# Optimization experiments

Measured on AMD Instinct MI355X. Metric: run time of the kernel, lower is better.

## Reference

```python
import jax, jax.numpy as jnp
import numpy as np

EPS_BN = 1e-5
K_NN = 5


def _curvature(x, k=K_NN):
    # x: [B, P, 3] -> concat inverse mean kNN distance -> [B, P, 4]
    def per_sample(pts):  # [P, 3]
        sq = jnp.sum(pts * pts, axis=1)
        d2 = sq[:, None] + sq[None, :] - 2.0 * (pts @ pts.T)
        dist = jnp.sqrt(jnp.maximum(d2, 0.0))  # [P, P], matches torch.cdist p=2
        neg_vals, _ = jax.lax.top_k(-dist, k + 1)  # k+1 smallest distances
        dists = -neg_vals[:, 1:]  # drop self (distance 0)
        dmean = jnp.mean(dists, axis=1, keepdims=True)  # [P, 1]
        return 1.0 / (1e-8 + dmean)
    curv = jax.vmap(per_sample)(x)  # [B, P, 1]
    return jnp.concatenate([x, curv], axis=2)


def _bn(h, g, b, axes):
    # BatchNorm (training mode, batch statistics), biased variance like torch
    m = jnp.mean(h, axis=axes, keepdims=True)
    v = jnp.var(h, axis=axes, keepdims=True)
    return (h - m) / jnp.sqrt(v + EPS_BN) * g + b


def setup_inputs() -> dict:
    key = jax.random.key(0)
    ks = jax.random.split(key, 16)
    B, P, OUTDIM = 32, 2048, 40

    def rn(k, shape, scale=0.05):
        return jax.random.normal(k, shape, dtype=jnp.float32) * scale

    return {
        "x": jax.random.normal(ks[0], (B, P, 3), dtype=jnp.float32),
        # 1x1 Conv1d weights stored as [out_ch, in_ch]
        "conv1_w": rn(ks[1], (64, 4)), "conv1_b": rn(ks[2], (64,)),
        "bn1_g": jnp.ones((64,), jnp.float32), "bn1_b": jnp.zeros((64,), jnp.float32),
        "conv2_w": rn(ks[3], (128, 64)), "conv2_b": rn(ks[4], (128,)),
        "bn2_g": jnp.ones((128,), jnp.float32), "bn2_b": jnp.zeros((128,), jnp.float32),
        "conv3_w": rn(ks[5], (1024, 128)), "conv3_b": rn(ks[6], (1024,)),
        "bn3_g": jnp.ones((1024,), jnp.float32), "bn3_b": jnp.zeros((1024,), jnp.float32),
        "fc1_w": rn(ks[7], (512, 1024)), "fc1_b": rn(ks[8], (512,)),
        "bnf1_g": jnp.ones((512,), jnp.float32), "bnf1_b": jnp.zeros((512,), jnp.float32),
        "fc2_w": rn(ks[9], (256, 512)), "fc2_b": rn(ks[10], (256,)),
        "bnf2_g": jnp.ones((256,), jnp.float32), "bnf2_b": jnp.zeros((256,), jnp.float32),
        # outdim separate Linear(256,1) layers stacked into one [OUTDIM, 256] matrix
        "out_w": rn(ks[11], (OUTDIM, 256)), "out_b": rn(ks[12], (OUTDIM,)),
    }


def reference(x, conv1_w, conv1_b, bn1_g, bn1_b, conv2_w, conv2_b, bn2_g, bn2_b,
              conv3_w, conv3_b, bn3_g, bn3_b, fc1_w, fc1_b, bnf1_g, bnf1_b,
              fc2_w, fc2_b, bnf2_g, bnf2_b, out_w, out_b):
    h = _curvature(x)  # [B, P, 4]
    # feature_layer1: Conv1d(4,64,1)+BN+ReLU; 1x1 conv == per-point matmul
    h = jax.nn.relu(_bn(h @ conv1_w.T + conv1_b, bn1_g, bn1_b, (0, 1)))
    # feature_layer2: Conv1d(64,128,1)+BN+ReLU, Conv1d(128,1024,1)+BN+ReLU
    h = jax.nn.relu(_bn(h @ conv2_w.T + conv2_b, bn2_g, bn2_b, (0, 1)))
    h = jax.nn.relu(_bn(h @ conv3_w.T + conv3_b, bn3_g, bn3_b, (0, 1)))
    h = jnp.max(h, axis=1)  # global max pool over points -> [B, 1024]
    # shared_layer
    h = jax.nn.relu(_bn(h @ fc1_w.T + fc1_b, bnf1_g, bnf1_b, (0,)))
    h = jax.nn.relu(_bn(h @ fc2_w.T + fc2_b, bnf2_g, bnf2_b, (0,)))
    logits = h @ out_w.T + out_b  # concatenated per-class Linear(256,1) heads
    return jax.nn.log_softmax(logits, axis=1)
```

## Files before the change

kernel.cpp:

```cpp
#include <hip/hip_runtime.h>
#include <hip/hip_bf16.h>
#include <math.h>

#define EPS_BN 1e-5f

constexpr int BATCH = 32;
constexpr int NPTS  = 2048;
constexpr int BP    = BATCH * NPTS;

using s16x8 = __attribute__((ext_vector_type(8))) short;
using u32x4 = __attribute__((ext_vector_type(4))) unsigned;
using f32x4 = __attribute__((ext_vector_type(4))) float;

static __device__ __forceinline__ unsigned short f2bf(float f) {
  union { float f; unsigned u; } x{f};
  unsigned r = x.u + 0x7fffu + ((x.u >> 16) & 1u);
  return (unsigned short)(r >> 16);
}
static __device__ __forceinline__ float bf2f(unsigned short s) {
  union { unsigned u; float f; } x;
  x.u = ((unsigned)s) << 16;
  return x.f;
}
static __device__ __forceinline__ unsigned pk2bf(float lo, float hi) {
  __hip_bfloat162 t = __float22bfloat162_rn(float2{lo, hi});
  unsigned r;
  __builtin_memcpy(&r, &t, 4);
  return r;
}

static __device__ __forceinline__ void gload_lds16(const void* g, void* l) {
  __builtin_amdgcn_global_load_lds((const __attribute__((address_space(1))) void*)g,
                                   (__attribute__((address_space(3))) void*)l, 16, 0, 0);
}

static __device__ __forceinline__ float wave_reduce_add(float v) {
#pragma unroll
  for (int off = 32; off > 0; off >>= 1) v += __shfl_xor(v, off);
  return v;
}

static __device__ __forceinline__ void ins6(float (&nn)[6], float c) {
  float b0 = fminf(nn[0], c);
  float b1 = __builtin_amdgcn_fmed3f(c, nn[1], nn[0]);
  float b2 = __builtin_amdgcn_fmed3f(c, nn[2], nn[1]);
  float b3 = __builtin_amdgcn_fmed3f(c, nn[3], nn[2]);
  float b4 = __builtin_amdgcn_fmed3f(c, nn[4], nn[3]);
  float b5 = __builtin_amdgcn_fmed3f(c, nn[5], nn[4]);
  nn[0] = b0; nn[1] = b1; nn[2] = b2; nn[3] = b3; nn[4] = b4; nn[5] = b5;
}

constexpr int CH = 260;
__global__ __launch_bounds__(256) void curv_kernel(const float* __restrict__ x,
                                                   float* __restrict__ feat) {
  __shared__ float sx[8 * CH], sy[8 * CH], sz[8 * CH], sh[8 * CH];
  int b = blockIdx.y;
  const float* xb = x + (size_t)b * NPTS * 3;
  int tid = threadIdx.x;
#pragma unroll
  for (int k = 0; k < 8; k++) {
    int i = k * 256 + tid;
    float qx = xb[i * 3 + 0], qy = xb[i * 3 + 1], qz = xb[i * 3 + 2];
    sx[k * CH + tid] = qx;
    sy[k * CH + tid] = qy;
    sz[k * CH + tid] = qz;
    sh[k * CH + tid] = 0.5f * (qx * qx + qy * qy + qz * qz);
  }
  __syncthreads();
  int row = blockIdx.x * 32 + (tid >> 3);
  int sub = tid & 7;
  float px = sx[(row >> 8) * CH + (row & 255)];
  float py = sy[(row >> 8) * CH + (row & 255)];
  float pz = sz[(row >> 8) * CH + (row & 255)];
  float nn[6];
#pragma unroll
  for (int j = 0; j < 6; j++) nn[j] = 3.4e38f;
  const float4* cx = (const float4*)(sx + sub * CH);
  const float4* cy = (const float4*)(sy + sub * CH);
  const float4* cz = (const float4*)(sz + sub * CH);
  const float4* chq = (const float4*)(sh + sub * CH);
  for (int j = 0; j < 64; j++) {
    float4 qx = cx[j], qy = cy[j], qz = cz[j], qh = chq[j];
    ins6(nn, fmaf(-px, qx.x, fmaf(-py, qy.x, fmaf(-pz, qz.x, qh.x))));
    ins6(nn, fmaf(-px, qx.y, fmaf(-py, qy.y, fmaf(-pz, qz.y, qh.y))));
    ins6(nn, fmaf(-px, qx.z, fmaf(-py, qy.z, fmaf(-pz, qz.z, qh.z))));
    ins6(nn, fmaf(-px, qx.w, fmaf(-py, qy.w, fmaf(-pz, qz.w, qh.w))));
  }
#pragma unroll
  for (int m = 1; m <= 4; m <<= 1) {
    float other[6];
#pragma unroll
    for (int k = 0; k < 6; k++) other[k] = __shfl_xor(nn[k], m);
#pragma unroll
    for (int k = 0; k < 6; k++) ins6(nn, other[k]);
  }
  if (sub == 0) {
    float p2 = px * px + py * py + pz * pz;
    float dm = 0.f;
#pragma unroll
    for (int i = 1; i < 6; i++) dm += sqrtf(fmaxf(fmaf(2.f, nn[i], p2), 0.f));
    dm *= 0.2f;
    float curv = 1.0f / (1e-8f + dm);
    size_t o = ((size_t)b * NPTS + row) * 4;
    feat[o + 0] = px;
    feat[o + 1] = py;
    feat[o + 2] = pz;
    feat[o + 3] = curv;
  }
}

__global__ __launch_bounds__(256) void gemm1s_kernel(const float* __restrict__ feat,
                                                     const float* __restrict__ w,
                                                     const float* __restrict__ bias,
                                                     unsigned short* __restrict__ z1bf,
                                                     float* __restrict__ part) {
  __shared__ float wT[4 * 64];
  int tid = threadIdx.x;
  { int k = tid >> 6, c = tid & 63; wT[k * 64 + c] = w[c * 4 + k]; }
  __syncthreads();
  int col = tid & 63, rg = tid >> 6;
  int row0 = blockIdx.x * 64;
  float w0 = wT[col], w1 = wT[64 + col], w2v = wT[128 + col], w3 = wT[192 + col];
  float bb = bias[col];
  float s = 0.f, q = 0.f;
  for (int i = 0; i < 16; i++) {
    int row = row0 + i * 4 + rg;
    const float4 f = *(const float4*)(feat + (size_t)row * 4);
    float acc = bb + f.x * w0 + f.y * w1 + f.z * w2v + f.w * w3;
    s += acc;
    q += acc * acc;
    z1bf[(size_t)row * 64 + col] = f2bf(acc);
  }
  __shared__ float ls[256], lq[256];
  ls[tid] = s; lq[tid] = q;
  __syncthreads();
  if (tid < 64) {
    float ss = 0.f, qq = 0.f;
#pragma unroll
    for (int i = 0; i < 4; i++) { ss += ls[i * 64 + tid]; qq += lq[i * 64 + tid]; }
    part[((size_t)blockIdx.x * 64 + tid) * 2 + 0] = ss;
    part[((size_t)blockIdx.x * 64 + tid) * 2 + 1] = qq;
  }
}

template <int C, int P>
__global__ __launch_bounds__(256) void bnfinP_kernel(const float* __restrict__ part,
                                                     const float* __restrict__ g,
                                                     const float* __restrict__ be,
                                                     float* __restrict__ scale,
                                                     float* __restrict__ shift) {
  int c = blockIdx.x, tid = threadIdx.x;
  float s = 0.f, q = 0.f;
  for (int i = tid; i < P; i += 256) {
    s += part[((size_t)i * C + c) * 2 + 0];
    q += part[((size_t)i * C + c) * 2 + 1];
  }
  __shared__ float ls[256], lq[256];
  ls[tid] = s; lq[tid] = q;
  __syncthreads();
  for (int off = 128; off > 0; off >>= 1) {
    if (tid < off) { ls[tid] += ls[tid + off]; lq[tid] += lq[tid + off]; }
    __syncthreads();
  }
  if (tid == 0) {
    float m = ls[0] * (1.0f / 65536.0f);
    float v = lq[0] * (1.0f / 65536.0f) - m * m;
    float a = g[c] / sqrtf(v + EPS_BN);
    scale[c] = a;
    shift[c] = be[c] - m * a;
  }
}

__global__ __launch_bounds__(256) void gemm2_mfma_kernel(const unsigned short* __restrict__ z1bf,
                                                         const float* __restrict__ s1,
                                                         const float* __restrict__ h1,
                                                         const float* __restrict__ w2,
                                                         const float* __restrict__ bias2,
                                                         unsigned short* __restrict__ z2bf,
                                                         float* __restrict__ part2) {
  __shared__ char lds[33280];
  float* ls1 = (float*)(lds + 32768);
  float* lh1 = ls1 + 64;
  int tid = threadIdx.x;
  int row0 = blockIdx.x * 128;
  if (tid < 64) { ls1[tid] = s1[tid]; lh1[tid] = h1[tid]; }

  s16x8 araw[4];
  float4 b0[4], b1[4];
#pragma unroll
  for (int i = 0; i < 4; i++) {
    int L = tid + 256 * i;
    araw[i] = *(const s16x8*)(z1bf + (size_t)row0 * 64 + (size_t)L * 8);
    int crow = L >> 3, k0 = (L & 7) * 8;
    b0[i] = *(const float4*)(w2 + (size_t)crow * 64 + k0);
    b1[i] = *(const float4*)(w2 + (size_t)crow * 64 + k0 + 4);
  }
  __syncthreads();

#pragma unroll
  for (int i = 0; i < 4; i++) {
    int L = tid + 256 * i;
    int row = L >> 3, grp = L & 7, k0 = grp * 8;
    float4 sA = *(const float4*)(ls1 + k0);
    float4 sB = *(const float4*)(ls1 + k0 + 4);
    float4 hA = *(const float4*)(lh1 + k0);
    float4 hB = *(const float4*)(lh1 + k0 + 4);
    float v0 = fmaxf(bf2f((unsigned short)araw[i][0]) * sA.x + hA.x, 0.f);
    float v1 = fmaxf(bf2f((unsigned short)araw[i][1]) * sA.y + hA.y, 0.f);
    float v2 = fmaxf(bf2f((unsigned short)araw[i][2]) * sA.z + hA.z, 0.f);
    float v3 = fmaxf(bf2f((unsigned short)araw[i][3]) * sA.w + hA.w, 0.f);
    float v4 = fmaxf(bf2f((unsigned short)araw[i][4]) * sB.x + hB.x, 0.f);
    float v5 = fmaxf(bf2f((unsigned short)araw[i][5]) * sB.y + hB.y, 0.f);
    float v6 = fmaxf(bf2f((unsigned short)araw[i][6]) * sB.z + hB.z, 0.f);
    float v7 = fmaxf(bf2f((unsigned short)araw[i][7]) * sB.w + hB.w, 0.f);
    u32x4 pa = {pk2bf(v0, v1), pk2bf(v2, v3), pk2bf(v4, v5), pk2bf(v6, v7)};
    *(u32x4*)(lds + row * 128 + ((grp ^ (row & 7)) << 4)) = pa;
    u32x4 pb = {pk2bf(b0[i].x, b0[i].y), pk2bf(b0[i].z, b0[i].w),
                pk2bf(b1[i].x, b1[i].y), pk2bf(b1[i].z, b1[i].w)};
    *(u32x4*)(lds + 16384 + row * 128 + ((grp ^ (row & 7)) << 4)) = pb;
  }
  __syncthreads();

  int w = tid >> 6, lane = tid & 63;
  int wm = w >> 1, wn = w & 1;
  int lrow = lane & 15, lg = lane >> 4;
  int sw = (lrow & 7) << 4;
  f32x4 acc[4][4] = {};
#pragma unroll
  for (int kstep = 0; kstep < 2; kstep++) {
    s16x8 a[4], bfr[4];
#pragma unroll
    for (int m = 0; m < 4; m++) {
      int row = wm * 64 + m * 16 + lrow;
      int byte = row * 128 + ((kstep * 64 + lg * 16) ^ sw);
      a[m] = *(const s16x8*)(lds + byte);
    }
#pragma unroll
    for (int n = 0; n < 4; n++) {
      int col = wn * 64 + n * 16 + lrow;
      int byte = 16384 + col * 128 + ((kstep * 64 + lg * 16) ^ sw);
      bfr[n] = *(const s16x8*)(lds + byte);
    }
#pragma unroll
    for (int m = 0; m < 4; m++)
#pragma unroll
      for (int n = 0; n < 4; n++)
        acc[m][n] = __builtin_amdgcn_mfma_f32_16x16x32_bf16(a[m], bfr[n], acc[m][n], 0, 0, 0);
  }
  __syncthreads();

  float* sS = (float*)lds;
  float* sQ = sS + 256;
#pragma unroll
  for (int n = 0; n < 4; n++) {
    int col = wn * 64 + n * 16 + lrow;
    float bb = bias2[col];
    float s = 0.f, q = 0.f;
#pragma unroll
    for (int m = 0; m < 4; m++) {
#pragma unroll
      for (int r = 0; r < 4; r++) {
        float v = acc[m][n][r] + bb;
        s += v;
        q += v * v;
        int row = row0 + wm * 64 + m * 16 + lg * 4 + r;
        z2bf[(size_t)row * 128 + col] = f2bf(v);
      }
    }
    s += __shfl_xor(s, 16); s += __shfl_xor(s, 32);
    q += __shfl_xor(q, 16); q += __shfl_xor(q, 32);
    if (lane < 16) {
      int cidx = wn * 64 + n * 16 + lane;
      sS[wm * 128 + cidx] = s;
      sQ[wm * 128 + cidx] = q;
    }
  }
  __syncthreads();
  if (tid < 128) {
    part2[((size_t)blockIdx.x * 128 + tid) * 2 + 0] = sS[tid] + sS[128 + tid];
    part2[((size_t)blockIdx.x * 128 + tid) * 2 + 1] = sQ[tid] + sQ[128 + tid];
  }
}

__global__ __launch_bounds__(256) void wconv_kernel(const float* __restrict__ w,
                                                    unsigned short* __restrict__ wbf) {
  int g = blockIdx.x * 256 + threadIdx.x;
  const float4 v = ((const float4*)w)[g];
  unsigned short o0 = f2bf(v.x), o1 = f2bf(v.y), o2 = f2bf(v.z), o3 = f2bf(v.w);
  unsigned short* d = wbf + (size_t)g * 4;
  d[0] = o0; d[1] = o1; d[2] = o2; d[3] = o3;
}

__global__ __launch_bounds__(256) void gemm3_mfma_kernel(const unsigned short* __restrict__ z2bf,
                                                         const float* __restrict__ s2,
                                                         const float* __restrict__ h2,
                                                         const unsigned short* __restrict__ wbf,
                                                         const float* __restrict__ bias3,
                                                         float* __restrict__ pS,
                                                         float* __restrict__ pQ,
                                                         float* __restrict__ pMx,
                                                         float* __restrict__ pMn) {
  __shared__ char lds[70656];
  float* ls2 = (float*)(lds + 69632);
  float* lh2 = ls2 + 128;
  int tid = threadIdx.x;
  int w = tid >> 6, lane = tid & 63;
  int bid = blockIdx.x;
  int rblk = (bid & 7) * 64 + (bid >> 3);
  int row0 = rblk * 128;

  if (tid < 128) { ls2[tid] = s2[tid]; lh2[tid] = h2[tid]; }
  s16x8 araw[8];
#pragma unroll
  for (int i = 0; i < 8; i++) {
    int L = tid + 256 * i;
    int row = L >> 4, gc = L & 15;
    araw[i] = *(const s16x8*)(z2bf + (size_t)(row0 + row) * 128 + gc * 8);
  }
  __syncthreads();
#pragma unroll
  for (int i = 0; i < 8; i++) {
    int L = tid + 256 * i;
    int row = L >> 4, gc = L & 15, k0 = gc * 8;
    float4 sA = *(const float4*)(ls2 + k0);
    float4 sB = *(const float4*)(ls2 + k0 + 4);
    float4 hA = *(const float4*)(lh2 + k0);
    float4 hB = *(const float4*)(lh2 + k0 + 4);
    float v0 = fmaxf(bf2f((unsigned short)araw[i][0]) * sA.x + hA.x, 0.f);
    float v1 = fmaxf(bf2f((unsigned short)araw[i][1]) * sA.y + hA.y, 0.f);
    float v2 = fmaxf(bf2f((unsigned short)araw[i][2]) * sA.z + hA.z, 0.f);
    float v3 = fmaxf(bf2f((unsigned short)araw[i][3]) * sA.w + hA.w, 0.f);
    float v4 = fmaxf(bf2f((unsigned short)araw[i][4]) * sB.x + hB.x, 0.f);
    float v5 = fmaxf(bf2f((unsigned short)araw[i][5]) * sB.y + hB.y, 0.f);
    float v6 = fmaxf(bf2f((unsigned short)araw[i][6]) * sB.z + hB.z, 0.f);
    float v7 = fmaxf(bf2f((unsigned short)araw[i][7]) * sB.w + hB.w, 0.f);
    u32x4 pa = {pk2bf(v0, v1), pk2bf(v2, v3), pk2bf(v4, v5), pk2bf(v6, v7)};
    *(u32x4*)(lds + row * 256 + ((gc ^ (row & 7)) << 4)) = pa;
  }

  int wm = w >> 1, wn = w & 1;
  int lrow = lane & 15, lg = lane >> 4;
  int sw = (lrow & 7) << 4;
  float* sS = (float*)(lds + 65536);
  float* sQ = sS + 256;
  float* sMx = sQ + 256;
  float* sMn = sMx + 256;

  for (int cblk = 0; cblk < 8; cblk++) {
    int col0 = cblk * 128;
#pragma unroll
    for (int i = 0; i < 8; i++) {
      int ldsoff = w * 8192 + i * 1024;
      int lin = ldsoff + lane * 16;
      int row = lin >> 8;
      int gc = (lin >> 4) & 15;
      int gcl = gc ^ (row & 7);
      gload_lds16(wbf + (size_t)(col0 + row) * 128 + gcl * 8, &lds[32768 + ldsoff]);
    }
    __syncthreads();

    f32x4 acc[4][4] = {};
#pragma unroll
    for (int kstep = 0; kstep < 4; kstep++) {
      s16x8 a[4], b[4];
#pragma unroll
      for (int m = 0; m < 4; m++) {
        int row = wm * 64 + m * 16 + lrow;
        int byte = row * 256 + ((kstep * 64 + lg * 16) ^ sw);
        a[m] = *(const s16x8*)(lds + byte);
      }
#pragma unroll
      for (int n = 0; n < 4; n++) {
        int col = wn * 64 + n * 16 + lrow;
        int byte = 32768 + col * 256 + ((kstep * 64 + lg * 16) ^ sw);
        b[n] = *(const s16x8*)(lds + byte);
      }
#pragma unroll
      for (int m = 0; m < 4; m++)
#pragma unroll
        for (int n = 0; n < 4; n++)
          acc[m][n] = __builtin_amdgcn_mfma_f32_16x16x32_bf16(a[m], b[n], acc[m][n], 0, 0, 0);
    }

#pragma unroll
    for (int n = 0; n < 4; n++) {
      float bb = bias3[col0 + wn * 64 + n * 16 + lrow];
      float s = 0.f, q = 0.f, mx = -3.4e38f, mn = 3.4e38f;
#pragma unroll
      for (int m = 0; m < 4; m++)
#pragma unroll
        for (int r = 0; r < 4; r++) {
          float v = acc[m][n][r] + bb;
          s += v;
          q += v * v;
          mx = fmaxf(mx, v);
          mn = fminf(mn, v);
        }
      s += __shfl_xor(s, 16); s += __shfl_xor(s, 32);
      q += __shfl_xor(q, 16); q += __shfl_xor(q, 32);
      mx = fmaxf(mx, __shfl_xor(mx, 16)); mx = fmaxf(mx, __shfl_xor(mx, 32));
      mn = fminf(mn, __shfl_xor(mn, 16)); mn = fminf(mn, __shfl_xor(mn, 32));
      if (lane < 16) {
        int cidx = wn * 64 + n * 16 + lane;
        sS[wm * 128 + cidx] = s;
        sQ[wm * 128 + cidx] = q;
        sMx[wm * 128 + cidx] = mx;
        sMn[wm * 128 + cidx] = mn;
      }
    }
    __syncthreads();
    if (tid < 128) {
      size_t o = (size_t)rblk * 1024 + col0 + tid;
      pS[o] = sS[tid] + sS[128 + tid];
      pQ[o] = sQ[tid] + sQ[128 + tid];
      pMx[o] = fmaxf(sMx[tid], sMx[128 + tid]);
      pMn[o] = fminf(sMn[tid], sMn[128 + tid]);
    }
    __syncthreads();
  }
}

__global__ __launch_bounds__(256) void bn3fin_pool_kernel(const float* __restrict__ pS,
                                                          const float* __restrict__ pQ,
                                                          const float* __restrict__ pMx,
                                                          const float* __restrict__ pMn,
                                                          const float* __restrict__ g,
                                                          const float* __restrict__ be,
                                                          float* __restrict__ pooled) {
  int tid = threadIdx.x;
  int chl = tid & 15, grp = tid >> 4;
  int c = blockIdx.x * 16 + chl;
  float s = 0.f, q = 0.f;
  for (int i = grp; i < 512; i += 16) {
    s += pS[(size_t)i * 1024 + c];
    q += pQ[(size_t)i * 1024 + c];
  }
  __shared__ float ls[256], lq[256], sa[16], sc[16];
  ls[chl * 16 + grp] = s;
  lq[chl * 16 + grp] = q;
  __syncthreads();
  if (tid < 16) {
    float ss = 0.f, qq = 0.f;
#pragma unroll
    for (int i = 0; i < 16; i++) { ss += ls[tid * 16 + i]; qq += lq[tid * 16 + i]; }
    float m = ss * (1.0f / 65536.0f);
    float v = qq * (1.0f / 65536.0f) - m * m;
    float a = g[blockIdx.x * 16 + tid] / sqrtf(v + EPS_BN);
    sa[tid] = a;
    sc[tid] = be[blockIdx.x * 16 + tid] - m * a;
  }
  __syncthreads();
  for (int idx = tid; idx < 512; idx += 256) {
    int b = idx >> 4, l = idx & 15;
    int cc = blockIdx.x * 16 + l;
    float mx = -3.4e38f, mn = 3.4e38f;
    for (int i = 0; i < 16; i++) {
      mx = fmaxf(mx, pMx[(size_t)(b * 16 + i) * 1024 + cc]);
      mn = fminf(mn, pMn[(size_t)(b * 16 + i) * 1024 + cc]);
    }
    float a = sa[l];
    float v = (a > 0.f) ? (a * mx + sc[l]) : (a * mn + sc[l]);
    pooled[(size_t)b * 1024 + cc] = fmaxf(v, 0.f);
  }
}

__global__ __launch_bounds__(256) void fc1_kernel(const float* __restrict__ pooled,
                                                  const float* __restrict__ w,
                                                  const float* __restrict__ bias,
                                                  float* __restrict__ zf1) {
  int gw = blockIdx.x * 4 + (threadIdx.x >> 6);
  int lane = threadIdx.x & 63;
  int b = gw >> 9, o = gw & 511;
  const float4* pr = (const float4*)(pooled + (size_t)b * 1024);
  const float4* wr = (const float4*)(w + (size_t)o * 1024);
  float acc = 0.f;
#pragma unroll
  for (int i = 0; i < 4; i++) {
    int k = lane + i * 64;
    float4 p = pr[k], q = wr[k];
    acc += p.x * q.x + p.y * q.y + p.z * q.z + p.w * q.w;
  }
  acc = wave_reduce_add(acc);
  if (lane == 0) zf1[gw] = acc + bias[o];
}

__global__ __launch_bounds__(256) void statsF_kernel(const float* __restrict__ z,
                                                     const float* __restrict__ g,
                                                     const float* __restrict__ be, int C,
                                                     float* __restrict__ scale,
                                                     float* __restrict__ shift) {
  int c = blockIdx.x * 256 + threadIdx.x;
  if (c >= C) return;
  float s = 0.f, q = 0.f;
  for (int b = 0; b < 32; b++) {
    float v = z[(size_t)b * C + c];
    s += v;
    q += v * v;
  }
  float m = s * (1.0f / 32.0f);
  float v = q * (1.0f / 32.0f) - m * m;
  float a = g[c] / sqrtf(v + EPS_BN);
  scale[c] = a;
  shift[c] = be[c] - m * a;
}

__global__ __launch_bounds__(256) void fc2_kernel(const float* __restrict__ zf1,
                                                  const float* __restrict__ sf1,
                                                  const float* __restrict__ hf1,
                                                  const float* __restrict__ w,
                                                  const float* __restrict__ bias,
                                                  float* __restrict__ zf2) {
  int gw = blockIdx.x * 4 + (threadIdx.x >> 6);
  int lane = threadIdx.x & 63;
  int b = gw >> 8, o = gw & 255;
  const float4* zr = (const float4*)(zf1 + (size_t)b * 512);
  const float4* sr = (const float4*)sf1;
  const float4* hr = (const float4*)hf1;
  const float4* wr = (const float4*)(w + (size_t)o * 512);
  float acc = 0.f;
#pragma unroll
  for (int i = 0; i < 2; i++) {
    int k = lane + i * 64;
    float4 z = zr[k], s = sr[k], h = hr[k], q = wr[k];
    float v0 = fmaxf(z.x * s.x + h.x, 0.f);
    float v1 = fmaxf(z.y * s.y + h.y, 0.f);
    float v2 = fmaxf(z.z * s.z + h.z, 0.f);
    float v3 = fmaxf(z.w * s.w + h.w, 0.f);
    acc += v0 * q.x + v1 * q.y + v2 * q.z + v3 * q.w;
  }
  acc = wave_reduce_add(acc);
  if (lane == 0) zf2[gw] = acc + bias[o];
}

__global__ __launch_bounds__(256) void head_kernel(const float* __restrict__ zf2,
                                                   const float* __restrict__ gf2,
                                                   const float* __restrict__ bef2,
                                                   const float* __restrict__ w,
                                                   const float* __restrict__ bias,
                                                   float* __restrict__ out) {
  int b = blockIdx.x, tid = threadIdx.x;
  int wv = tid >> 6, lane = tid & 63;
  __shared__ float ssf[256], shf[256], lg[40], red[2];
  {
    float s = 0.f, q = 0.f;
    for (int bb = 0; bb < 32; bb++) {
      float v = zf2[(size_t)bb * 256 + tid];
      s += v;
      q += v * v;
    }
    float m = s * (1.0f / 32.0f);
    float var = q * (1.0f / 32.0f) - m * m;
    float a = gf2[tid] / sqrtf(var + EPS_BN);
    ssf[tid] = a;
    shf[tid] = bef2[tid] - m * a;
  }
  __syncthreads();
  float4 z = ((const float4*)(zf2 + (size_t)b * 256))[lane];
  float4 s = ((const float4*)ssf)[lane];
  float4 h = ((const float4*)shf)[lane];
  float v0 = fmaxf(z.x * s.x + h.x, 0.f);
  float v1 = fmaxf(z.y * s.y + h.y, 0.f);
  float v2 = fmaxf(z.z * s.z + h.z, 0.f);
  float v3 = fmaxf(z.w * s.w + h.w, 0.f);
  for (int r = 0; r < 10; r++) {
    int o = wv * 10 + r;
    float4 q = ((const float4*)(w + (size_t)o * 256))[lane];
    float a = v0 * q.x + v1 * q.y + v2 * q.z + v3 * q.w;
    a = wave_reduce_add(a);
    if (lane == 0) lg[o] = a + bias[o];
  }
  __syncthreads();
  if (tid == 0) {
    float mx = -3.4e38f;
    for (int i = 0; i < 40; i++) mx = fmaxf(mx, lg[i]);
    float sum = 0.f;
    for (int i = 0; i < 40; i++) sum += expf(lg[i] - mx);
    red[0] = mx;
    red[1] = logf(sum);
  }
  __syncthreads();
  if (tid < 40) out[(size_t)b * 40 + tid] = lg[tid] - red[0] - red[1];
}

extern "C" void kernel_launch(void* const* d_in, const int* in_sizes, int n_in,
                              void* d_out, int out_size, void* d_ws, size_t ws_size,
                              hipStream_t stream) {
  const float* x    = (const float*)d_in[0];
  const float* c1w  = (const float*)d_in[1];
  const float* c1b  = (const float*)d_in[2];
  const float* g1   = (const float*)d_in[3];
  const float* be1  = (const float*)d_in[4];
  const float* c2w  = (const float*)d_in[5];
  const float* c2b  = (const float*)d_in[6];
  const float* g2   = (const float*)d_in[7];
  const float* be2  = (const float*)d_in[8];
  const float* c3w  = (const float*)d_in[9];
  const float* c3b  = (const float*)d_in[10];
  const float* g3   = (const float*)d_in[11];
  const float* be3  = (const float*)d_in[12];
  const float* f1w  = (const float*)d_in[13];
  const float* f1b  = (const float*)d_in[14];
  const float* gf1  = (const float*)d_in[15];
  const float* bef1 = (const float*)d_in[16];
  const float* f2w  = (const float*)d_in[17];
  const float* f2b  = (const float*)d_in[18];
  const float* gf2  = (const float*)d_in[19];
  const float* bef2 = (const float*)d_in[20];
  const float* ow   = (const float*)d_in[21];
  const float* ob   = (const float*)d_in[22];
  float* out = (float*)d_out;

  float* W = (float*)d_ws;
  float* feat   = W;
  float* pS     = feat + 262144;
  float* pQ     = pS + 524288;
  float* pMx    = pQ + 524288;
  float* pMn    = pMx + 524288;
  float* part   = pMn + 524288;
  float* part2  = part + 131072;
  float* pooled = part2 + 131072;
  float* zf1    = pooled + 32768;
  float* zf2    = zf1 + 16384;
  float* s1     = zf2 + 8192;
  float* h1     = s1 + 64;
  float* s2     = h1 + 64;
  float* h2     = s2 + 128;
  float* sf1    = h2 + 128;
  float* hf1    = sf1 + 512;
  unsigned short* wbf  = (unsigned short*)(hf1 + 512);
  unsigned short* z1bf = wbf + 131072;
  unsigned short* z2bf = z1bf + (size_t)BP * 64;

  wconv_kernel<<<128, 256, 0, stream>>>(c3w, wbf);
  curv_kernel<<<dim3(64, 32), 256, 0, stream>>>(x, feat);
  gemm1s_kernel<<<1024, 256, 0, stream>>>(feat, c1w, c1b, z1bf, part);
  bnfinP_kernel<64, 1024><<<64, 256, 0, stream>>>(part, g1, be1, s1, h1);
  gemm2_mfma_kernel<<<512, 256, 0, stream>>>(z1bf, s1, h1, c2w, c2b, z2bf, part2);
  bnfinP_kernel<128, 512><<<128, 256, 0, stream>>>(part2, g2, be2, s2, h2);
  gemm3_mfma_kernel<<<512, 256, 0, stream>>>(z2bf, s2, h2, wbf, c3b, pS, pQ, pMx, pMn);
  bn3fin_pool_kernel<<<64, 256, 0, stream>>>(pS, pQ, pMx, pMn, g3, be3, pooled);
  fc1_kernel<<<4096, 256, 0, stream>>>(pooled, f1w, f1b, zf1);
  statsF_kernel<<<2, 256, 0, stream>>>(zf1, gf1, bef1, 512, sf1, hf1);
  fc2_kernel<<<2048, 256, 0, stream>>>(zf1, sf1, hf1, f2w, f2b, zf2);
  head_kernel<<<32, 256, 0, stream>>>(zf2, gf2, bef2, ow, ob, out);
}
```

Measured before the change: 133.6 us.

## Fuse curvature with conv1 and hoist conv3 bias out of epilogue stats

Merges the curvature kernel with the first 1x1 conv and its BN partial statistics. The features stay in shared memory and the global feat buffer round trip plus one launch go away. The number of partial-stat blocks doubles, so the BN1 finalize reads twice as many partials. In gemm3's epilogue the per-column bias is applied after the reduction by algebraically adjusting the sum, sum of squares, max and min. This removes a per-element add but may change float rounding slightly.

```diff
diff --git a/kernel.cpp b/kernel.cpp
--- a/kernel.cpp
+++ b/kernel.cpp
@@ -51,12 +51,22 @@
 }
 
 constexpr int CH = 260;
-__global__ __launch_bounds__(256) void curv_kernel(const float* __restrict__ x,
-                                                   float* __restrict__ feat) {
+__global__ __launch_bounds__(256) void curv1_kernel(const float* __restrict__ x,
+                                                    const float* __restrict__ c1w,
+                                                    const float* __restrict__ c1b,
+                                                    unsigned short* __restrict__ z1bf,
+                                                    float* __restrict__ part) {
   __shared__ float sx[8 * CH], sy[8 * CH], sz[8 * CH], sh[8 * CH];
+  __shared__ float wT[4 * 64], lb1[64], sfeat[32 * 4];
+  __shared__ float ls[256], lq[256];
   int b = blockIdx.y;
   const float* xb = x + (size_t)b * NPTS * 3;
   int tid = threadIdx.x;
+  {
+    int k = tid >> 6, c = tid & 63;
+    wT[k * 64 + c] = c1w[c * 4 + k];
+    if (tid < 64) lb1[tid] = c1b[tid];
+  }
 #pragma unroll
   for (int k = 0; k < 8; k++) {
     int i = k * 256 + tid;
@@ -101,45 +111,39 @@
     for (int i = 1; i < 6; i++) dm += sqrtf(fmaxf(fmaf(2.f, nn[i], p2), 0.f));
     dm *= 0.2f;
     float curv = 1.0f / (1e-8f + dm);
-    size_t o = ((size_t)b * NPTS + row) * 4;
-    feat[o + 0] = px;
-    feat[o + 1] = py;
-    feat[o + 2] = pz;
-    feat[o + 3] = curv;
-  }
-}
-
-__global__ __launch_bounds__(256) void gemm1s_kernel(const float* __restrict__ feat,
-                                                     const float* __restrict__ w,
-                                                     const float* __restrict__ bias,
-                                                     unsigned short* __restrict__ z1bf,
-                                                     float* __restrict__ part) {
-  __shared__ float wT[4 * 64];
-  int tid = threadIdx.x;
-  { int k = tid >> 6, c = tid & 63; wT[k * 64 + c] = w[c * 4 + k]; }
-  __syncthreads();
-  int col = tid & 63, rg = tid >> 6;
-  int row0 = blockIdx.x * 64;
-  float w0 = wT[col], w1 = wT[64 + col], w2v = wT[128 + col], w3 = wT[192 + col];
-  float bb = bias[col];
-  float s = 0.f, q = 0.f;
-  for (int i = 0; i < 16; i++) {
-    int row = row0 + i * 4 + rg;
-    const float4 f = *(const float4*)(feat + (size_t)row * 4);
-    float acc = bb + f.x * w0 + f.y * w1 + f.z * w2v + f.w * w3;
-    s += acc;
-    q += acc * acc;
-    z1bf[(size_t)row * 64 + col] = f2bf(acc);
-  }
-  __shared__ float ls[256], lq[256];
-  ls[tid] = s; lq[tid] = q;
+    int lr = tid >> 3;
+    sfeat[lr * 4 + 0] = px;
+    sfeat[lr * 4 + 1] = py;
+    sfeat[lr * 4 + 2] = pz;
+    sfeat[lr * 4 + 3] = curv;
+  }
+  __syncthreads();
+  {
+    int c = tid & 63, rg = tid >> 6;
+    float w0 = wT[c], w1 = wT[64 + c], w2v = wT[128 + c], w3 = wT[192 + c];
+    float bb = lb1[c];
+    int growbase = b * NPTS + blockIdx.x * 32;
+    float s = 0.f, q = 0.f;
+#pragma unroll
+    for (int i = 0; i < 8; i++) {
+      int lr = rg * 8 + i;
+      float4 f = *(const float4*)(sfeat + lr * 4);
+      float acc = bb + f.x * w0 + f.y * w1 + f.z * w2v + f.w * w3;
+      s += acc;
+      q += acc * acc;
+      z1bf[(size_t)(growbase + lr) * 64 + c] = f2bf(acc);
+    }
+    ls[tid] = s;
+    lq[tid] = q;
+  }
   __syncthreads();
   if (tid < 64) {
     float ss = 0.f, qq = 0.f;
 #pragma unroll
     for (int i = 0; i < 4; i++) { ss += ls[i * 64 + tid]; qq += lq[i * 64 + tid]; }
-    part[((size_t)blockIdx.x * 64 + tid) * 2 + 0] = ss;
-    part[((size_t)blockIdx.x * 64 + tid) * 2 + 1] = qq;
+    size_t bid = (size_t)b * 64 + blockIdx.x;
+    part[(bid * 64 + tid) * 2 + 0] = ss;
+    part[(bid * 64 + tid) * 2 + 1] = qq;
   }
 }
 
@@ -384,15 +388,14 @@
 
 #pragma unroll
     for (int n = 0; n < 4; n++) {
-      float bb = bias3[col0 + wn * 64 + n * 16 + lrow];
       float s = 0.f, q = 0.f, mx = -3.4e38f, mn = 3.4e38f;
 #pragma unroll
       for (int m = 0; m < 4; m++)
 #pragma unroll
         for (int r = 0; r < 4; r++) {
-          float v = acc[m][n][r] + bb;
+          float v = acc[m][n][r];
           s += v;
-          q += v * v;
+          q = fmaf(v, v, q);
           mx = fmaxf(mx, v);
           mn = fminf(mn, v);
         }
@@ -410,11 +413,14 @@
     }
     __syncthreads();
     if (tid < 128) {
+      float bcol = bias3[col0 + tid];
+      float S = sS[tid] + sS[128 + tid];
+      float Q = sQ[tid] + sQ[128 + tid];
       size_t o = (size_t)rblk * 1024 + col0 + tid;
-      pS[o] = sS[tid] + sS[128 + tid];
-      pQ[o] = sQ[tid] + sQ[128 + tid];
-      pMx[o] = fmaxf(sMx[tid], sMx[128 + tid]);
-      pMn[o] = fminf(sMn[tid], sMn[128 + tid]);
+      pS[o] = S + 128.f * bcol;
+      pQ[o] = Q + 2.f * bcol * S + 128.f * bcol * bcol;
+      pMx[o] = fmaxf(sMx[tid], sMx[128 + tid]) + bcol;
+      pMn[o] = fminf(sMn[tid], sMn[128 + tid]) + bcol;
     }
     __syncthreads();
   }
@@ -611,13 +617,12 @@
   float* out = (float*)d_out;
 
   float* W = (float*)d_ws;
-  float* feat   = W;
-  float* pS     = feat + 262144;
+  float* pS     = W;
   float* pQ     = pS + 524288;
   float* pMx    = pQ + 524288;
   float* pMn    = pMx + 524288;
   float* part   = pMn + 524288;
-  float* part2  = part + 131072;
+  float* part2  = part + 262144;
   float* pooled = part2 + 131072;
   float* zf1    = pooled + 32768;
   float* zf2    = zf1 + 16384;
@@ -632,9 +637,8 @@
   unsigned short* z2bf = z1bf + (size_t)BP * 64;
 
   wconv_kernel<<<128, 256, 0, stream>>>(c3w, wbf);
-  curv_kernel<<<dim3(64, 32), 256, 0, stream>>>(x, feat);
-  gemm1s_kernel<<<1024, 256, 0, stream>>>(feat, c1w, c1b, z1bf, part);
-  bnfinP_kernel<64, 1024><<<64, 256, 0, stream>>>(part, g1, be1, s1, h1);
+  curv1_kernel<<<dim3(64, 32), 256, 0, stream>>>(x, c1w, c1b, z1bf, part);
+  bnfinP_kernel<64, 2048><<<64, 256, 0, stream>>>(part, g1, be1, s1, h1);
   gemm2_mfma_kernel<<<512, 256, 0, stream>>>(z1bf, s1, h1, c2w, c2b, z2bf, part2);
   bnfinP_kernel<128, 512><<<128, 256, 0, stream>>>(part2, g2, be2, s2, h2);
   gemm3_mfma_kernel<<<512, 256, 0, stream>>>(z2bf, s2, h2, wbf, c3b, pS, pQ, pMx, pMn);
```

Result: faster. 130.6 us (-2.2%).
